# Performance work log

Hardware: AMD Instinct MI355X
Metric: run time of the kernel (lower is better)

## Reference

```python
import jax, jax.numpy as jnp
import numpy as np
from jax import lax

B, T = 8192, 128
HID = 64


def setup_inputs() -> dict:
    key = jax.random.key(0)
    ks = jax.random.split(key, 16)
    actor_ids = jax.random.randint(ks[0], (B, T), 0, 7, dtype=jnp.int32)
    action_ids = jax.random.randint(ks[1], (B, T), 0, 4, dtype=jnp.int32)
    street_ids = jax.random.randint(ks[2], (B, T), 0, 5, dtype=jnp.int32)
    bet_fraction = jax.random.uniform(ks[3], (B, T, 1), dtype=jnp.float32)
    # prefix-valid mask from random lengths (some zero-length rows)
    lengths = jax.random.randint(ks[4], (B,), 0, T + 1)
    valid_mask = jnp.arange(T)[None, :] < lengths[:, None]  # [B,T] bool
    s = 0.1
    params = {
        "E_actor": jax.random.normal(ks[5], (7, 8), jnp.float32) * s,
        "E_action": jax.random.normal(ks[6], (4, 8), jnp.float32) * s,
        "E_street": jax.random.normal(ks[7], (5, 4), jnp.float32) * s,
        "W_proj": jax.random.normal(ks[8], (32, 21), jnp.float32) * s,
        "b_proj": jax.random.normal(ks[9], (32,), jnp.float32) * s,
        "W_ih": jax.random.normal(ks[10], (3 * HID, 32), jnp.float32) * s,
        "W_hh": jax.random.normal(ks[11], (3 * HID, HID), jnp.float32) * s,
        "b_ih": jax.random.normal(ks[12], (3 * HID,), jnp.float32) * s,
        "b_hh": jax.random.normal(ks[13], (3 * HID,), jnp.float32) * s,
    }
    return dict(actor_ids=actor_ids, action_ids=action_ids, street_ids=street_ids,
                bet_fraction=bet_fraction, valid_mask=valid_mask, **params)


def reference(actor_ids, action_ids, street_ids, bet_fraction, valid_mask,
              E_actor, E_action, E_street, W_proj, b_proj,
              W_ih, W_hh, b_ih, b_hh):
    # embed + concat -> [B,T,21]
    feats = jnp.concatenate([E_actor[actor_ids], E_action[action_ids],
                             E_street[street_ids], bet_fraction], axis=-1)
    x = feats @ W_proj.T + b_proj                      # [B,T,32]
    # precompute input-side GRU gates for all timesteps: [B,T,3H]
    xg = x @ W_ih.T + b_ih
    xg_t = jnp.swapaxes(xg, 0, 1)                      # [T,B,3H]
    m_t = jnp.swapaxes(valid_mask, 0, 1)               # [T,B]

    def step(h, inp):
        xg_i, m = inp
        hg = h @ W_hh.T + b_hh                         # [B,3H]
        xr, xz, xn = jnp.split(xg_i, 3, axis=-1)
        hr, hz, hn = jnp.split(hg, 3, axis=-1)
        r = jax.nn.sigmoid(xr + hr)
        z = jax.nn.sigmoid(xz + hz)
        n = jnp.tanh(xn + r * hn)
        h_new = (1.0 - z) * n + z * h
        # only advance hidden state while t < length (prefix-valid mask);
        # final carry equals the GRU hidden at the last valid step, and rows
        # with length 0 stay at the zero init (matches torch masking).
        h = jnp.where(m[:, None], h_new, h)
        return h, None

    h0 = jnp.zeros((x.shape[0], HID), dtype=x.dtype)
    h_final, _ = lax.scan(step, h0, (xg_t, m_t))
    return h_final
```

## Files before the change

### kernel.cpp

```cpp
#include <hip/hip_runtime.h>

#define HID 64
#define TT  128
#define NROWS 8192
#define NGRP (NROWS / 16)
#define LOG2E 1.44269504088896f

typedef _Float16 half8 __attribute__((ext_vector_type(8)));
typedef float    f32x4 __attribute__((ext_vector_type(4)));


__global__ void k_len(const int* __restrict__ mask, int* __restrict__ lens) {
    const int row = blockIdx.x * 4 + (threadIdx.x >> 6);
    const int l   = threadIdx.x & 63;
    const int* mrow = mask + row * TT;
    int c = (mrow[l] != 0) + (mrow[l + 64] != 0);
    #pragma unroll
    for (int k = 32; k >= 1; k >>= 1) c += __shfl_xor(c, k);
    if (l == 0) lens[row] = c;
}

__global__ __launch_bounds__(1024) void k_sort(const int* __restrict__ lens,
                                               int* __restrict__ perm) {
    __shared__ int hist[TT + 1];
    __shared__ int offs[TT + 1];
    const int tid = threadIdx.x;
    if (tid <= TT) hist[tid] = 0;
    __syncthreads();
    int myL[8];
    #pragma unroll
    for (int i = 0; i < 8; i++) {
        myL[i] = lens[tid + 1024 * i];
        atomicAdd(&hist[myL[i]], 1);
    }
    __syncthreads();
    if (tid <= TT) {
        int s = 0;
        for (int j = 0; j < tid; j++) s += hist[j];
        offs[tid] = s;
    }
    __syncthreads();
    #pragma unroll
    for (int i = 0; i < 8; i++) {
        const int pos = atomicAdd(&offs[myL[i]], 1);
        const int d   = NROWS - 1 - pos;
        const int gd  = d >> 4, r = d & 15;
        const int b   = (gd < 256) ? gd : 767 - gd;
        perm[b * 16 + r] = tid + 1024 * i;
    }
}

__global__ __launch_bounds__(256, 2) void gru_fused(
    const int* __restrict__ actor_ids, const int* __restrict__ action_ids,
    const int* __restrict__ street_ids, const float* __restrict__ bet,
    const float* __restrict__ E_actor, const float* __restrict__ E_action,
    const float* __restrict__ E_street, const float* __restrict__ W_proj,
    const float* __restrict__ b_proj, const float* __restrict__ W_ih,
    const float* __restrict__ b_ih, const float* __restrict__ W_hh,
    const float* __restrict__ b_hh, const int* __restrict__ perm,
    const int* __restrict__ lens, float* __restrict__ out)
{
    __shared__ __align__(16) union {
        float wfs[192][32];
        struct {
            int pb[TT][17];
            __align__(16) _Float16 hb[2][16][72];
            int Lsh[16];
            int Psh[16];
        } c;
    } A;
    __shared__ __align__(16) _Float16 embl[144];
    __shared__ float bfs[192];

    const int tid = threadIdx.x;
    const int wv  = tid >> 6;
    const int l   = tid & 63;
    const int q   = l >> 4;
    const int n   = l & 15;
    const int g   = blockIdx.x;

    for (int i = tid; i < 136; i += 256) {
        int r = i >> 3, m = i & 7;
        float v = 0.f;
        if (r < 7)       v = E_actor[r * 8 + m];
        else if (r < 11) v = E_action[(r - 7) * 8 + m];
        else if (r < 16) v = (m < 4) ? E_street[(r - 11) * 4 + m] : 0.f;
        embl[i] = (_Float16)v;
    }

    if (tid < 192) {
        const int j = tid;
        float wf[21];
        #pragma unroll
        for (int m = 0; m < 21; m++) wf[m] = 0.f;
        float bf = b_ih[j];
        for (int k = 0; k < 32; k++) {
            const float w = W_ih[j * 32 + k];
            bf += w * b_proj[k];
            #pragma unroll
            for (int m = 0; m < 21; m++) wf[m] += w * W_proj[k * 21 + m];
        }
        const float s = (j < 128) ? LOG2E : 2.f * LOG2E;
        #pragma unroll
        for (int m = 0; m < 21; m++) A.wfs[j][m] = wf[m] * s;
        #pragma unroll
        for (int m = 21; m < 32; m++) A.wfs[j][m] = 0.f;
        bfs[j] = bf;
    }
    __syncthreads();

    half8 Af[3], Ah[3][2];
    {
        const int m16 = l & 15, kq = l >> 4;
        #pragma unroll
        for (int g3 = 0; g3 < 3; g3++) {
            const int jr = g3 * 64 + wv * 16 + m16;
            _Float16 v[8];
            #pragma unroll
            for (int m = 0; m < 8; m++) v[m] = (_Float16)A.wfs[jr][kq * 8 + m];
            Af[g3] = *(half8*)v;
            const float s = (g3 < 2) ? LOG2E : 2.f * LOG2E;
            #pragma unroll
            for (int kt = 0; kt < 2; kt++) {
                _Float16 w[8];
                #pragma unroll
                for (int m = 0; m < 8; m++)
                    w[m] = (_Float16)(W_hh[jr * HID + kt * 32 + kq * 8 + m] * s);
                Ah[g3][kt] = *(half8*)w;
            }
        }
    }
    f32x4 biasR, biasZ, biasX, biasH;
    #pragma unroll
    for (int e = 0; e < 4; e++) {
        const int idx = 16 * wv + 4 * q + e;
        biasR[e] = (bfs[idx]      + b_hh[idx])      * LOG2E;
        biasZ[e] = (bfs[64 + idx] + b_hh[64 + idx]) * LOG2E;
        biasX[e] = bfs[128 + idx]  * (2.f * LOG2E);
        biasH[e] = b_hh[128 + idx] * (2.f * LOG2E);
    }
    __syncthreads();

    for (int i = tid; i < 2 * 16 * 72 / 2; i += 256) ((int*)A.c.hb)[i] = 0;
    {
        const int r = tid >> 4, tl = tid & 15;
        const int prow = perm[g * 16 + r];
        const int base = prow * TT;
        #pragma unroll
        for (int i = 0; i < 8; i++) {
            const int t = tl + 16 * i;
            const int a = actor_ids[base + t], c = action_ids[base + t];
            const int s = street_ids[base + t];
            const _Float16 f16 = (_Float16)bet[base + t];
            const unsigned fb = (unsigned)*(const unsigned short*)&f16;
            A.c.pb[t][r] = (int)(a | (c << 3) | (s << 5) | (fb << 16));
        }
        if (tl == 0) { A.c.Lsh[r] = lens[prow]; A.c.Psh[r] = prow; }
    }
    __syncthreads();

    const int Ln = A.c.Lsh[n];
    int Lmax = Ln;
    #pragma unroll
    for (int k = 1; k < 16; k <<= 1) {
        const int o = __shfl_xor(Lmax, k);
        Lmax = (o > Lmax) ? o : Lmax;
    }

    const bool isq2 = (q == 2);
    const int sh = (q == 1) ? 3 : (q == 2) ? 5 : 0;
    const int mk = (q == 1) ? 3 : (q == 3) ? 0 : 7;
    const int of = (q == 1) ? 7 : (q == 2) ? 11 : (q == 3) ? 16 : 0;

    float h[4] = {0.f, 0.f, 0.f, 0.f};
    const f32x4 zero4 = {0.f, 0.f, 0.f, 0.f};

    f32x4 xR, xZ, xX;
    {
        const int p = A.c.pb[0][n];
        const int eidx = ((p >> sh) & mk) + of;
        half8 Bf = *(const half8*)&embl[eidx * 8];
        uint4* bu = (uint4*)&Bf;
        bu->z = isq2 ? ((unsigned)p >> 16) : bu->z;
        xR = __builtin_amdgcn_mfma_f32_16x16x32_f16(Af[0], Bf, biasR, 0, 0, 0);
        xZ = __builtin_amdgcn_mfma_f32_16x16x32_f16(Af[1], Bf, biasZ, 0, 0, 0);
        xX = __builtin_amdgcn_mfma_f32_16x16x32_f16(Af[2], Bf, biasX, 0, 0, 0);
    }

    for (int t = 0; t < Lmax; t++) {
        const int buf = t & 1;
        const half8 Bh0 = *(const half8*)&A.c.hb[buf][n][q * 8];
        const half8 Bh1 = *(const half8*)&A.c.hb[buf][n][32 + q * 8];
        f32x4 aRa = __builtin_amdgcn_mfma_f32_16x16x32_f16(Ah[0][0], Bh0, xR, 0, 0, 0);
        f32x4 aRb = __builtin_amdgcn_mfma_f32_16x16x32_f16(Ah[0][1], Bh1, zero4, 0, 0, 0);
        f32x4 aZ = __builtin_amdgcn_mfma_f32_16x16x32_f16(Ah[1][0], Bh0, xZ, 0, 0, 0);
        aZ = __builtin_amdgcn_mfma_f32_16x16x32_f16(Ah[1][1], Bh1, aZ, 0, 0, 0);
        f32x4 aH = __builtin_amdgcn_mfma_f32_16x16x32_f16(Ah[2][0], Bh0, biasH, 0, 0, 0);
        aH = __builtin_amdgcn_mfma_f32_16x16x32_f16(Ah[2][1], Bh1, aH, 0, 0, 0);
        const f32x4 aR = aRa + aRb;
        const f32x4 aXc = xX;

        {
            const int tn = (t + 1 < TT) ? t + 1 : TT - 1;
            const int p = A.c.pb[tn][n];
            const int eidx = ((p >> sh) & mk) + of;
            half8 Bf = *(const half8*)&embl[eidx * 8];
            uint4* bu = (uint4*)&Bf;
            bu->z = isq2 ? ((unsigned)p >> 16) : bu->z;
            xR = __builtin_amdgcn_mfma_f32_16x16x32_f16(Af[0], Bf, biasR, 0, 0, 0);
            xZ = __builtin_amdgcn_mfma_f32_16x16x32_f16(Af[1], Bf, biasZ, 0, 0, 0);
            xX = __builtin_amdgcn_mfma_f32_16x16x32_f16(Af[2], Bf, biasX, 0, 0, 0);
        }

        const bool live = (t < Ln);
        _Float16 hp[4];
        #pragma unroll
        for (int e = 0; e < 4; e++) {
            const float r = __builtin_amdgcn_rcpf(1.f + __builtin_amdgcn_exp2f(-aR[e]));
            const float z = __builtin_amdgcn_rcpf(1.f + __builtin_amdgcn_exp2f(-aZ[e]));
            const float y2 = aXc[e] + r * aH[e];
            const float nn = 1.f - 2.f * __builtin_amdgcn_rcpf(1.f + __builtin_amdgcn_exp2f(y2));
            const float hv = nn + z * (h[e] - nn);
            h[e] = live ? hv : h[e];
            hp[e] = (_Float16)h[e];
        }
        *(uint2*)&A.c.hb[buf ^ 1][n][16 * wv + 4 * q] = *(uint2*)hp;
        __syncthreads();
    }

    const int prow = A.c.Psh[n];
    float4 o = make_float4(h[0], h[1], h[2], h[3]);
    *(float4*)&out[prow * HID + 16 * wv + 4 * q] = o;
}

extern "C" void kernel_launch(void* const* d_in, const int* in_sizes, int n_in,
                              void* d_out, int out_size, void* d_ws, size_t ws_size,
                              hipStream_t stream) {
    const int*   actor_ids  = (const int*)d_in[0];
    const int*   action_ids = (const int*)d_in[1];
    const int*   street_ids = (const int*)d_in[2];
    const float* bet        = (const float*)d_in[3];
    const int*   vmask      = (const int*)d_in[4];
    const float* E_actor    = (const float*)d_in[5];
    const float* E_action   = (const float*)d_in[6];
    const float* E_street   = (const float*)d_in[7];
    const float* W_proj     = (const float*)d_in[8];
    const float* b_proj     = (const float*)d_in[9];
    const float* W_ih       = (const float*)d_in[10];
    const float* W_hh       = (const float*)d_in[11];
    const float* b_ih       = (const float*)d_in[12];
    const float* b_hh       = (const float*)d_in[13];
    float*       out        = (float*)d_out;

    int* ws   = (int*)d_ws;
    int* lens = ws;
    int* perm = ws + NROWS;

    k_len<<<NROWS / 4, 256, 0, stream>>>(vmask, lens);
    k_sort<<<1, 1024, 0, stream>>>(lens, perm);

    gru_fused<<<NGRP, 256, 0, stream>>>(actor_ids, action_ids, street_ids, bet,
                                        E_actor, E_action, E_street,
                                        W_proj, b_proj, W_ih, b_ih, W_hh, b_hh,
                                        perm, lens, out);
}
```

Before: 166.5 us.

## Make each wave own four rows to remove per-step block barriers

Shrinks the GRU block to 128 threads, and each wave now computes all 192 gates for 4 sequences. The hidden state stays wave-private, so the per-timestep __syncthreads is gone. The input bias is folded into the projection weights through a constant-one input column, and the input-gate MFMA is prefetched two steps ahead. The sort permutation is adjusted to 8-row groups. The cost is much more redundant MFMA work per row and a large register footprint, and the pb writes and reads rely on intra-wave ordering without a barrier.

```diff
diff --git a/kernel.cpp b/kernel.cpp
--- a/kernel.cpp
+++ b/kernel.cpp
@@ -3,7 +3,7 @@
 #define HID 64
 #define TT  128
 #define NROWS 8192
-#define NGRP (NROWS / 16)
+#define NGRP (NROWS / 8)
 #define LOG2E 1.44269504088896f
 
 typedef _Float16 half8 __attribute__((ext_vector_type(8)));
@@ -44,13 +44,17 @@
     for (int i = 0; i < 8; i++) {
         const int pos = atomicAdd(&offs[myL[i]], 1);
         const int d   = NROWS - 1 - pos;
-        const int gd  = d >> 4, r = d & 15;
-        const int b   = (gd < 256) ? gd : 767 - gd;
-        perm[b * 16 + r] = tid + 1024 * i;
-    }
-}
-
-__global__ __launch_bounds__(256, 2) void gru_fused(
+        const int g8  = d >> 3, r = d & 7;
+        int b;
+        if      (g8 < 256) b = g8;
+        else if (g8 < 512) b = 256 + (511 - g8);
+        else if (g8 < 768) b = 512 + (g8 - 512);
+        else               b = 768 + (1023 - g8);
+        perm[b * 8 + r] = tid + 1024 * i;
+    }
+}
+
+__global__ __launch_bounds__(128, 2) void gru_fused(
     const int* __restrict__ actor_ids, const int* __restrict__ action_ids,
     const int* __restrict__ street_ids, const float* __restrict__ bet,
     const float* __restrict__ E_actor, const float* __restrict__ E_action,
@@ -61,25 +65,27 @@
     const int* __restrict__ lens, float* __restrict__ out)
 {
     __shared__ __align__(16) union {
-        float wfs[192][32];
+        _Float16 wfs[192][32];
         struct {
-            int pb[TT][17];
-            __align__(16) _Float16 hb[2][16][72];
-            int Lsh[16];
-            int Psh[16];
+            int pb[TT][9];
+            __align__(16) _Float16 hb[8][80];
+            int Lsh[8];
+            int Psh[8];
         } c;
     } A;
     __shared__ __align__(16) _Float16 embl[144];
-    __shared__ float bfs[192];
 
     const int tid = threadIdx.x;
-    const int wv  = tid >> 6;
+    const int wid = tid >> 6;
     const int l   = tid & 63;
-    const int q   = l >> 4;
-    const int n   = l & 15;
+    const int u   = l >> 4;
+    const int cc  = l & 15;
+    const int cr4 = cc & 3;
+    const int rep = cc >> 2;
+    const int gr  = 4 * wid + cr4;
     const int g   = blockIdx.x;
 
-    for (int i = tid; i < 136; i += 256) {
+    for (int i = tid; i < 136; i += 128) {
         int r = i >> 3, m = i & 7;
         float v = 0.f;
         if (r < 7)       v = E_actor[r * 8 + m];
@@ -88,8 +94,7 @@
         embl[i] = (_Float16)v;
     }
 
-    if (tid < 192) {
-        const int j = tid;
+    for (int j = tid; j < 192; j += 128) {
         float wf[21];
         #pragma unroll
         for (int m = 0; m < 21; m++) wf[m] = 0.f;
@@ -100,51 +105,42 @@
             #pragma unroll
             for (int m = 0; m < 21; m++) wf[m] += w * W_proj[k * 21 + m];
         }
+        if (j < 128) bf += b_hh[j];
         const float s = (j < 128) ? LOG2E : 2.f * LOG2E;
         #pragma unroll
-        for (int m = 0; m < 21; m++) A.wfs[j][m] = wf[m] * s;
-        #pragma unroll
-        for (int m = 21; m < 32; m++) A.wfs[j][m] = 0.f;
-        bfs[j] = bf;
-    }
-    __syncthreads();
-
-    half8 Af[3], Ah[3][2];
-    {
-        const int m16 = l & 15, kq = l >> 4;
-        #pragma unroll
-        for (int g3 = 0; g3 < 3; g3++) {
-            const int jr = g3 * 64 + wv * 16 + m16;
-            _Float16 v[8];
+        for (int m = 0; m < 21; m++) A.wfs[j][m] = (_Float16)(wf[m] * s);
+        A.wfs[j][21] = (_Float16)(bf * s);
+        #pragma unroll
+        for (int m = 22; m < 32; m++) A.wfs[j][m] = (_Float16)0.f;
+    }
+    __syncthreads();
+
+    half8 Af[12], Ah[12][2];
+    #pragma unroll
+    for (int jt = 0; jt < 12; jt++) {
+        const int jr = jt * 16 + cc;
+        Af[jt] = *(const half8*)&A.wfs[jr][u * 8];
+        const float s = (jt < 8) ? LOG2E : 2.f * LOG2E;
+        #pragma unroll
+        for (int kt = 0; kt < 2; kt++) {
+            _Float16 w8[8];
             #pragma unroll
-            for (int m = 0; m < 8; m++) v[m] = (_Float16)A.wfs[jr][kq * 8 + m];
-            Af[g3] = *(half8*)v;
-            const float s = (g3 < 2) ? LOG2E : 2.f * LOG2E;
-            #pragma unroll
-            for (int kt = 0; kt < 2; kt++) {
-                _Float16 w[8];
-                #pragma unroll
-                for (int m = 0; m < 8; m++)
-                    w[m] = (_Float16)(W_hh[jr * HID + kt * 32 + kq * 8 + m] * s);
-                Ah[g3][kt] = *(half8*)w;
-            }
-        }
-    }
-    f32x4 biasR, biasZ, biasX, biasH;
-    #pragma unroll
-    for (int e = 0; e < 4; e++) {
-        const int idx = 16 * wv + 4 * q + e;
-        biasR[e] = (bfs[idx]      + b_hh[idx])      * LOG2E;
-        biasZ[e] = (bfs[64 + idx] + b_hh[64 + idx]) * LOG2E;
-        biasX[e] = bfs[128 + idx]  * (2.f * LOG2E);
-        biasH[e] = b_hh[128 + idx] * (2.f * LOG2E);
-    }
-    __syncthreads();
-
-    for (int i = tid; i < 2 * 16 * 72 / 2; i += 256) ((int*)A.c.hb)[i] = 0;
+            for (int m = 0; m < 8; m++)
+                w8[m] = (_Float16)(W_hh[jr * HID + kt * 32 + u * 8 + m] * s);
+            Ah[jt][kt] = *(half8*)w8;
+        }
+    }
+    f32x4 biasH[4];
+    #pragma unroll
+    for (int T = 0; T < 4; T++)
+        #pragma unroll
+        for (int e = 0; e < 4; e++)
+            biasH[T][e] = b_hh[128 + 16 * T + 4 * u + e] * (2.f * LOG2E);
+    __syncthreads();
+
     {
         const int r = tid >> 4, tl = tid & 15;
-        const int prow = perm[g * 16 + r];
+        const int prow = perm[g * 8 + r];
         const int base = prow * TT;
         #pragma unroll
         for (int i = 0; i < 8; i++) {
@@ -157,60 +153,69 @@
         }
         if (tl == 0) { A.c.Lsh[r] = lens[prow]; A.c.Psh[r] = prow; }
     }
-    __syncthreads();
-
-    const int Ln = A.c.Lsh[n];
+
+    const int Ln = A.c.Lsh[gr];
     int Lmax = Ln;
-    #pragma unroll
-    for (int k = 1; k < 16; k <<= 1) {
-        const int o = __shfl_xor(Lmax, k);
-        Lmax = (o > Lmax) ? o : Lmax;
-    }
-
-    const bool isq2 = (q == 2);
-    const int sh = (q == 1) ? 3 : (q == 2) ? 5 : 0;
-    const int mk = (q == 1) ? 3 : (q == 3) ? 0 : 7;
-    const int of = (q == 1) ? 7 : (q == 2) ? 11 : (q == 3) ? 16 : 0;
-
+    { int o = __shfl_xor(Lmax, 1); Lmax = o > Lmax ? o : Lmax; }
+    { int o = __shfl_xor(Lmax, 2); Lmax = o > Lmax ? o : Lmax; }
+
+    _Float16* hbR = &A.c.hb[gr][0];
+    *(uint2*)&hbR[16 * rep + 4 * u] = make_uint2(0u, 0u);
+
+    const bool isu2 = (u == 2);
+    const int sh = (u == 1) ? 3 : (u == 2) ? 5 : 0;
+    const int mk = (u == 1) ? 3 : (u == 3) ? 0 : 7;
+    const int of = (u == 1) ? 7 : (u == 2) ? 11 : (u == 3) ? 16 : 0;
+
+    const f32x4 zero4 = {0.f, 0.f, 0.f, 0.f};
     float h[4] = {0.f, 0.f, 0.f, 0.f};
-    const f32x4 zero4 = {0.f, 0.f, 0.f, 0.f};
-
-    f32x4 xR, xZ, xX;
+
+    half8 Bf, Bfn;
     {
-        const int p = A.c.pb[0][n];
-        const int eidx = ((p >> sh) & mk) + of;
-        half8 Bf = *(const half8*)&embl[eidx * 8];
-        uint4* bu = (uint4*)&Bf;
-        bu->z = isq2 ? ((unsigned)p >> 16) : bu->z;
-        xR = __builtin_amdgcn_mfma_f32_16x16x32_f16(Af[0], Bf, biasR, 0, 0, 0);
-        xZ = __builtin_amdgcn_mfma_f32_16x16x32_f16(Af[1], Bf, biasZ, 0, 0, 0);
-        xX = __builtin_amdgcn_mfma_f32_16x16x32_f16(Af[2], Bf, biasX, 0, 0, 0);
+        const int p0 = A.c.pb[0][gr];
+        Bf = *(const half8*)&embl[(((p0 >> sh) & mk) + of) * 8];
+        uint4* b0 = (uint4*)&Bf;
+        b0->z = isu2 ? (((unsigned)p0 >> 16) | 0x3C000000u) : b0->z;
+        const int p1 = A.c.pb[1][gr];
+        Bfn = *(const half8*)&embl[(((p1 >> sh) & mk) + of) * 8];
+        uint4* b1 = (uint4*)&Bfn;
+        b1->z = isu2 ? (((unsigned)p1 >> 16) | 0x3C000000u) : b1->z;
     }
 
     for (int t = 0; t < Lmax; t++) {
-        const int buf = t & 1;
-        const half8 Bh0 = *(const half8*)&A.c.hb[buf][n][q * 8];
-        const half8 Bh1 = *(const half8*)&A.c.hb[buf][n][32 + q * 8];
-        f32x4 aRa = __builtin_amdgcn_mfma_f32_16x16x32_f16(Ah[0][0], Bh0, xR, 0, 0, 0);
-        f32x4 aRb = __builtin_amdgcn_mfma_f32_16x16x32_f16(Ah[0][1], Bh1, zero4, 0, 0, 0);
-        f32x4 aZ = __builtin_amdgcn_mfma_f32_16x16x32_f16(Ah[1][0], Bh0, xZ, 0, 0, 0);
-        aZ = __builtin_amdgcn_mfma_f32_16x16x32_f16(Ah[1][1], Bh1, aZ, 0, 0, 0);
-        f32x4 aH = __builtin_amdgcn_mfma_f32_16x16x32_f16(Ah[2][0], Bh0, biasH, 0, 0, 0);
-        aH = __builtin_amdgcn_mfma_f32_16x16x32_f16(Ah[2][1], Bh1, aH, 0, 0, 0);
-        const f32x4 aR = aRa + aRb;
-        const f32x4 aXc = xX;
-
+        const half8 Bh0 = *(const half8*)&hbR[8 * u];
+        const half8 Bh1 = *(const half8*)&hbR[32 + 8 * u];
+        const int t2 = (t + 2 < TT) ? t + 2 : TT - 1;
+        const int p2 = A.c.pb[t2][gr];
+
+        f32x4 x[12];
+        #pragma unroll
+        for (int jt = 0; jt < 12; jt++)
+            x[jt] = __builtin_amdgcn_mfma_f32_16x16x32_f16(Af[jt], Bf, zero4, 0, 0, 0);
+        f32x4 acc[8];
+        #pragma unroll
+        for (int jt = 0; jt < 8; jt++) {
+            f32x4 t0 = __builtin_amdgcn_mfma_f32_16x16x32_f16(Ah[jt][0], Bh0, x[jt], 0, 0, 0);
+            acc[jt]  = __builtin_amdgcn_mfma_f32_16x16x32_f16(Ah[jt][1], Bh1, t0, 0, 0, 0);
+        }
+        f32x4 hn[4];
+        #pragma unroll
+        for (int T = 0; T < 4; T++) {
+            f32x4 t0 = __builtin_amdgcn_mfma_f32_16x16x32_f16(Ah[8 + T][0], Bh0, biasH[T], 0, 0, 0);
+            hn[T]    = __builtin_amdgcn_mfma_f32_16x16x32_f16(Ah[8 + T][1], Bh1, t0, 0, 0, 0);
+        }
+
+        half8 Bf2;
         {
-            const int tn = (t + 1 < TT) ? t + 1 : TT - 1;
-            const int p = A.c.pb[tn][n];
-            const int eidx = ((p >> sh) & mk) + of;
-            half8 Bf = *(const half8*)&embl[eidx * 8];
-            uint4* bu = (uint4*)&Bf;
-            bu->z = isq2 ? ((unsigned)p >> 16) : bu->z;
-            xR = __builtin_amdgcn_mfma_f32_16x16x32_f16(Af[0], Bf, biasR, 0, 0, 0);
-            xZ = __builtin_amdgcn_mfma_f32_16x16x32_f16(Af[1], Bf, biasZ, 0, 0, 0);
-            xX = __builtin_amdgcn_mfma_f32_16x16x32_f16(Af[2], Bf, biasX, 0, 0, 0);
-        }
+            Bf2 = *(const half8*)&embl[(((p2 >> sh) & mk) + of) * 8];
+            uint4* b2 = (uint4*)&Bf2;
+            b2->z = isu2 ? (((unsigned)p2 >> 16) | 0x3C000000u) : b2->z;
+        }
+
+        const f32x4 aR  = rep < 2 ? (rep == 0 ? acc[0] : acc[1]) : (rep == 2 ? acc[2] : acc[3]);
+        const f32x4 aZ  = rep < 2 ? (rep == 0 ? acc[4] : acc[5]) : (rep == 2 ? acc[6] : acc[7]);
+        const f32x4 xn  = rep < 2 ? (rep == 0 ? x[8]   : x[9])   : (rep == 2 ? x[10]  : x[11]);
+        const f32x4 hnv = rep < 2 ? (rep == 0 ? hn[0]  : hn[1])  : (rep == 2 ? hn[2]  : hn[3]);
 
         const bool live = (t < Ln);
         _Float16 hp[4];
@@ -218,19 +223,19 @@
         for (int e = 0; e < 4; e++) {
             const float r = __builtin_amdgcn_rcpf(1.f + __builtin_amdgcn_exp2f(-aR[e]));
             const float z = __builtin_amdgcn_rcpf(1.f + __builtin_amdgcn_exp2f(-aZ[e]));
-            const float y2 = aXc[e] + r * aH[e];
+            const float y2 = xn[e] + r * hnv[e];
             const float nn = 1.f - 2.f * __builtin_amdgcn_rcpf(1.f + __builtin_amdgcn_exp2f(y2));
             const float hv = nn + z * (h[e] - nn);
             h[e] = live ? hv : h[e];
             hp[e] = (_Float16)h[e];
         }
-        *(uint2*)&A.c.hb[buf ^ 1][n][16 * wv + 4 * q] = *(uint2*)hp;
-        __syncthreads();
-    }
-
-    const int prow = A.c.Psh[n];
-    float4 o = make_float4(h[0], h[1], h[2], h[3]);
-    *(float4*)&out[prow * HID + 16 * wv + 4 * q] = o;
+        *(uint2*)&hbR[16 * rep + 4 * u] = *(uint2*)hp;
+
+        Bf = Bfn; Bfn = Bf2;
+    }
+
+    const int prow = A.c.Psh[gr];
+    *(float4*)&out[prow * HID + 16 * rep + 4 * u] = make_float4(h[0], h[1], h[2], h[3]);
 }
 
 extern "C" void kernel_launch(void* const* d_in, const int* in_sizes, int n_in,
@@ -259,7 +264,7 @@
     k_len<<<NROWS / 4, 256, 0, stream>>>(vmask, lens);
     k_sort<<<1, 1024, 0, stream>>>(lens, perm);
 
-    gru_fused<<<NGRP, 256, 0, stream>>>(actor_ids, action_ids, street_ids, bet,
+    gru_fused<<<NGRP, 128, 0, stream>>>(actor_ids, action_ids, street_ids, bet,
                                         E_actor, E_action, E_street,
                                         W_proj, b_proj, W_ih, b_ih, W_hh, b_hh,
                                         perm, lens, out);
```

After: 218.0 us. +30.9%, slower.
